# Optimization experiments

Measured on AMD Instinct MI355X. Metric: run time of the kernel, lower is better.

## Reference

```python
import jax, jax.numpy as jnp
import numpy as np

EPS = 1e-5  # torch InstanceNorm2d default eps

def instance_norm(x):
    # per-sample, per-channel normalization over spatial dims (affine=False)
    m = jnp.mean(x, axis=(2, 3), keepdims=True)
    v = jnp.var(x, axis=(2, 3), keepdims=True)
    return (x - m) * jax.lax.rsqrt(v + EPS)

def conv2d(x, w, b, stride, pad):
    y = jax.lax.conv_general_dilated(
        x, w, (stride, stride), [(pad, pad), (pad, pad)],
        dimension_numbers=('NCHW', 'OIHW', 'NCHW'))
    return y + b[None, :, None, None]

def res_block(x, w1, b1, w2, b2):
    out = conv2d(jax.nn.relu(instance_norm(x)), w1, b1, 1, 1)
    out = conv2d(jax.nn.relu(instance_norm(out)), w2, b2, 1, 1)
    return out + x

def res_block_strided(x, w1, b1, w2, b2, ws, bs):
    out = conv2d(jax.nn.relu(instance_norm(x)), w1, b1, 2, 1)
    out = conv2d(jax.nn.relu(instance_norm(out)), w2, b2, 1, 1)
    return out + conv2d(x, ws, bs, 2, 0)  # 1x1 strided skip projection

def setup_inputs() -> dict:
    key = jax.random.key(0)
    ks = jax.random.split(key, 12)
    B, N, C, H, W = 64, 1, 3, 256, 256
    TEXT, EMB, F, HEADS = 256, 512, 32, 5
    FH, FW = H // 16, W // 16  # 16, 16
    def rn(k, shape, scale=0.05):
        return jax.random.normal(k, shape, dtype=jnp.float32) * scale
    z = lambda *s: jnp.zeros(s, jnp.float32)
    return {
        'x': jax.random.normal(ks[0], (B, N, C, H, W), jnp.float32),
        'text_vector': jax.random.normal(ks[1], (B, TEXT), jnp.float32),
        'conv1_w': rn(ks[2], (F, C, 7, 7)),
        'conv1_b': z(F),
        'rbs_w1': rn(ks[3], (3, F, F, 3, 3)),  # 3 strided resblocks
        'rbs_b1': z(3, F),
        'rbs_w2': rn(ks[4], (3, F, F, 3, 3)),
        'rbs_b2': z(3, F),
        'rbs_ws': rn(ks[5], (3, F, F, 1, 1)),
        'rbs_bs': z(3, F),
        'rb_w1': rn(ks[6], (2, F, F, 3, 3)),  # 2 plain resblocks
        'rb_b1': z(2, F),
        'rb_w2': rn(ks[7], (2, F, F, 3, 3)),
        'rb_b2': z(2, F),
        'attn_w': rn(ks[8], (HEADS, FH * FW, TEXT)),  # torch Linear [out,in] per head
        'attn_b': z(HEADS, FH * FW),
        'final_w': rn(ks[9], (EMB, FH * FW * HEADS)),
        'final_b': z(EMB),
    }

def reference(x, text_vector, conv1_w, conv1_b, rbs_w1, rbs_b1, rbs_w2, rbs_b2,
              rbs_ws, rbs_bs, rb_w1, rb_b1, rb_w2, rb_b2, attn_w, attn_b,
              final_w, final_b):
    B, N, C, H, W = x.shape
    feat = x.reshape(B, N * C, H, W)
    feat = instance_norm(feat)
    feat = conv2d(feat, conv1_w, conv1_b, 2, 3)
    # block1 = strided + plain; block2 = strided + plain; block3 = strided
    feat = res_block_strided(feat, rbs_w1[0], rbs_b1[0], rbs_w2[0], rbs_b2[0], rbs_ws[0], rbs_bs[0])
    feat = res_block(feat, rb_w1[0], rb_b1[0], rb_w2[0], rb_b2[0])
    feat = res_block_strided(feat, rbs_w1[1], rbs_b1[1], rbs_w2[1], rbs_b2[1], rbs_ws[1], rbs_bs[1])
    feat = res_block(feat, rb_w1[1], rb_b1[1], rb_w2[1], rb_b2[1])
    feat = res_block_strided(feat, rbs_w1[2], rbs_b1[2], rbs_w2[2], rbs_b2[2], rbs_ws[2], rbs_bs[2])
    # feat: [B, 32, FH, FW]
    HEADS = attn_w.shape[0]
    FH, FW = feat.shape[2], feat.shape[3]
    # sigmoid-gated spatial attention logits per head: [B, HEADS, FH, FW]
    a = jax.nn.sigmoid(jnp.einsum('bt,hot->bho', text_vector, attn_w) + attn_b[None])
    a = a.reshape(B, HEADS, FH, FW)
    # channel scores: spatial sum of gate * feature -> [B, HEADS, C]
    scores = jnp.einsum('bhij,bcij->bhc', a, feat)
    probs = jax.nn.softmax(scores, axis=-1)  # old F.softmax over channel dim
    # weighted channel sum -> per-head attention map [B, HEADS, FH, FW]
    amaps = jnp.einsum('bhc,bcij->bhij', probs, feat)
    out = amaps.reshape(B, -1) @ final_w.T + final_b
    return out
```

## Files before the change

### kernel.cpp

```cpp
#include <hip/hip_runtime.h>
#include <cstdint>
#include <cstddef>

#define INORM_EPS 1e-5f

typedef _Float16 f16;
typedef f16 f16x8 __attribute__((ext_vector_type(8)));
typedef f16 f16x4 __attribute__((ext_vector_type(4)));
typedef float f32x4 __attribute__((ext_vector_type(4)));

__global__ __launch_bounds__(256) void prep(
    const float* __restrict__ rbs_w1, const float* __restrict__ rbs_w2,
    const float* __restrict__ rb_w1, const float* __restrict__ rb_w2,
    const float* __restrict__ rbs_ws, const float* __restrict__ conv1_w,
    float2* __restrict__ SP, f16* __restrict__ wp3, f16* __restrict__ wp1,
    f16* __restrict__ wp7) {
  int i = blockIdx.x * 256 + threadIdx.x;
  if (i < 20672) { SP[i] = make_float2(0.f, 0.f); return; }
  i -= 20672;
  if (i < 92160) {
    int mat = i / 9216, r = i % 9216;
    int p = r >> 10, f = (r >> 9) & 1, l = (r >> 3) & 63, j = r & 7;
    int co = f * 16 + (l & 15), ci = (l >> 4) * 8 + j;
    const float* src; int m;
    if (mat < 3) { src = rbs_w1; m = mat; }
    else if (mat < 6) { src = rbs_w2; m = mat - 3; }
    else if (mat < 8) { src = rb_w1; m = mat - 6; }
    else { src = rb_w2; m = mat - 8; }
    wp3[i] = (f16)src[m * 9216 + co * 288 + ci * 9 + p];
    return;
  }
  i -= 92160;
  if (i < 3072) {
    int mat = i / 1024, r = i % 1024;
    int f = r >> 9, l = (r >> 3) & 63, j = r & 7;
    wp1[i] = (f16)rbs_ws[mat * 1024 + (f * 16 + (l & 15)) * 32 + (l >> 4) * 8 + j];
    return;
  }
  i -= 3072;
  if (i >= 7168) return;
  int ky = i >> 10, f = (i >> 9) & 1, l = (i >> 3) & 63, j = i & 7;
  int k = (l >> 4) * 8 + j, kx = k >> 2, ci = k & 3;
  float v = 0.f;
  if (kx < 7 && ci < 3) v = conv1_w[(f * 16 + (l & 15)) * 147 + ci * 49 + ky * 7 + kx];
  wp7[i] = (f16)v;
}

__global__ __launch_bounds__(256) void stats_raw(const float* __restrict__ in,
                                                 float2* __restrict__ st, int HW) {
  const int map = blockIdx.x >> 3, chunk = blockIdx.x & 7;
  const int n4 = HW >> 5;
  const float4* p = (const float4*)(in + (size_t)map * HW + (size_t)chunk * (HW >> 3));
  float s = 0.f, ss = 0.f;
  for (int i = threadIdx.x; i < n4; i += 256) {
    float4 v = p[i];
    s += v.x + v.y + v.z + v.w;
    ss += v.x * v.x + v.y * v.y + v.z * v.z + v.w * v.w;
  }
  __shared__ float r0[256], r1[256];
  r0[threadIdx.x] = s;
  r1[threadIdx.x] = ss;
  __syncthreads();
  for (int off = 128; off > 0; off >>= 1) {
    if ((int)threadIdx.x < off) {
      r0[threadIdx.x] += r0[threadIdx.x + off];
      r1[threadIdx.x] += r1[threadIdx.x + off];
    }
    __syncthreads();
  }
  if (threadIdx.x == 0) {
    atomicAdd(&st[map].x, r0[0]);
    atomicAdd(&st[map].y, r1[0]);
  }
}

__global__ __launch_bounds__(256) void packx(const float* __restrict__ x,
                                             const float2* __restrict__ SPx,
                                             f16* __restrict__ xP) {
  int u = blockIdx.x * 256 + threadIdx.x;
  if (u >= 262 * 262) return;
  int b = blockIdx.z;
  int r = u / 262, c = u % 262;
  f16x4 out;
  out[0] = (f16)0; out[1] = (f16)0; out[2] = (f16)0; out[3] = (f16)0;
  if (r >= 3 && r < 259 && c >= 3 && c < 259) {
    int ir = r - 3, ic = c - 3;
#pragma unroll
    for (int ci = 0; ci < 3; ci++) {
      float2 s = SPx[b * 3 + ci];
      float mean = s.x * (1.f / 65536.f);
      float rstd = rsqrtf(s.y * (1.f / 65536.f) - mean * mean + INORM_EPS);
      out[ci] = (f16)((x[((size_t)b * 3 + ci) * 65536 + ir * 256 + ic] - mean) * rstd);
    }
  }
  *(f16x4*)(xP + ((size_t)b * 68644 + u) * 4) = out;
}

template <int W, int SKIP>
__global__ __launch_bounds__(256) void conv3r(
    const f16* __restrict__ Rin, const float2* __restrict__ SPin, float inv_hw,
    const f16* __restrict__ wp, const float* __restrict__ bias,
    const float* __restrict__ bias2, const f16* __restrict__ skip,
    const f16* __restrict__ wps, f16* __restrict__ Rout,
    float2* __restrict__ ostats) {
  constexpr int TPR = W / 16;
  constexpr int RPB = 8;
  constexpr int LEN = (RPB * TPR) / 4;
  const int t = threadIdx.x, w = t >> 6, l = t & 63;
  const int n = l & 15, q = l >> 4;
  const int b = blockIdx.z;
  const int tx = w % TPR;
  const int y0 = blockIdx.x * RPB + (w / TPR) * LEN;
  const int x = (tx << 4) + n;
  const f16* Rb = Rin + (size_t)b * W * W * 32;

  f16x8 sc, sh;
#pragma unroll
  for (int j = 0; j < 8; j++) {
    float2 s = SPin[b * 32 + q * 8 + j];
    float mean = s.x * inv_hw;
    float rstd = rsqrtf(s.y * inv_hw - mean * mean + INORM_EPS);
    sc[j] = (f16)rstd;
    sh[j] = (f16)(-mean * rstd);
  }

  f16x8 wf[18];
#pragma unroll
  for (int i = 0; i < 18; i++) wf[i] = *(const f16x8*)(wp + i * 512 + l * 8);
  f16x8 wsf0, wsf1;
  if (SKIP == 2) {
    wsf0 = *(const f16x8*)(wps + l * 8);
    wsf1 = *(const f16x8*)(wps + 512 + l * 8);
  }
  float b0 = bias[n], b1 = bias[16 + n];
  if (SKIP == 2) { b0 += bias2[n]; b1 += bias2[16 + n]; }

  f16* ro = Rout + (size_t)b * W * W * 32;
  const f16* sb = skip ? skip + (size_t)b * (SKIP == 2 ? 4 : 1) * W * W * 32 : nullptr;

  bool okc[3];
#pragma unroll
  for (int kx = 0; kx < 3; kx++) okc[kx] = (unsigned)(x + kx - 1) < (unsigned)W;

  auto rowload = [&](int gy, f16x8* dst) {
    int gyc = min(max(gy, 0), W - 1);
#pragma unroll
    for (int kx = 0; kx < 3; kx++) {
      int gxc = min(max(x + kx - 1, 0), W - 1);
      dst[kx] = *(const f16x8*)(Rb + ((size_t)gyc * W + gxc) * 32 + q * 8);
    }
  };
  auto rownorm = [&](int gy, const f16x8* src, f16x8* dst) {
    bool okr = (unsigned)gy < (unsigned)W;
#pragma unroll
    for (int kx = 0; kx < 3; kx++) {
      f16x8 v = src[kx] * sc + sh;
#pragma unroll
      for (int e = 0; e < 8; e++) v[e] = v[e] > (f16)0 ? v[e] : (f16)0;
      f16x8 z = {};
      dst[kx] = (okr && okc[kx]) ? v : z;
    }
  };

  float sm0 = 0.f, sq0 = 0.f, sm1 = 0.f, sq1 = 0.f;
  f16x8 win[9];
  f16x8 tmp[3], pf[3];
#pragma unroll
  for (int jj = 0; jj < 3; jj++) {
    rowload(y0 + jj - 1, tmp);
    rownorm(y0 + jj - 1, tmp, &win[jj * 3]);
  }

#pragma unroll
  for (int i = 0; i < LEN; i++) {
    int y = y0 + i;
    if (i + 1 < LEN) rowload(y0 + i + 2, pf);
    f32x4 acc0 = {0.f, 0.f, 0.f, 0.f}, acc1 = {0.f, 0.f, 0.f, 0.f};
#pragma unroll
    for (int ky = 0; ky < 3; ky++) {
      int slot = (i + ky) % 3;
#pragma unroll
      for (int kx = 0; kx < 3; kx++) {
        f16x8 a = win[slot * 3 + kx];
        acc0 = __builtin_amdgcn_mfma_f32_16x16x32_f16(a, wf[2 * (ky * 3 + kx)], acc0, 0, 0, 0);
        acc1 = __builtin_amdgcn_mfma_f32_16x16x32_f16(a, wf[2 * (ky * 3 + kx) + 1], acc1, 0, 0, 0);
      }
    }
    if (SKIP == 2) {
      const int Ws = 2 * W;
      f16x8 as = *(const f16x8*)(sb + ((size_t)(2 * y) * Ws + 2 * x) * 32 + q * 8);
      acc0 = __builtin_amdgcn_mfma_f32_16x16x32_f16(as, wsf0, acc0, 0, 0, 0);
      acc1 = __builtin_amdgcn_mfma_f32_16x16x32_f16(as, wsf1, acc1, 0, 0, 0);
    }
#pragma unroll
    for (int r = 0; r < 4; r++) {
      size_t px = (size_t)y * W + (tx << 4) + q * 4 + r;
      float v0 = acc0[r] + b0;
      float v1 = acc1[r] + b1;
      if (SKIP == 1) {
        v0 += (float)sb[px * 32 + n];
        v1 += (float)sb[px * 32 + 16 + n];
      }
      ro[px * 32 + n] = (f16)v0;
      ro[px * 32 + 16 + n] = (f16)v1;
      sm0 += v0; sq0 += v0 * v0;
      sm1 += v1; sq1 += v1 * v1;
    }
    if (i + 1 < LEN) rownorm(y0 + i + 2, pf, &win[(i % 3) * 3]);
  }
  if (ostats) {
    sm0 += __shfl_xor(sm0, 16); sm0 += __shfl_xor(sm0, 32);
    sq0 += __shfl_xor(sq0, 16); sq0 += __shfl_xor(sq0, 32);
    sm1 += __shfl_xor(sm1, 16); sm1 += __shfl_xor(sm1, 32);
    sq1 += __shfl_xor(sq1, 16); sq1 += __shfl_xor(sq1, 32);
    if (l < 16) {
      atomicAdd(&ostats[b * 32 + n].x, sm0);
      atomicAdd(&ostats[b * 32 + n].y, sq0);
      atomicAdd(&ostats[b * 32 + 16 + n].x, sm1);
      atomicAdd(&ostats[b * 32 + 16 + n].y, sq1);
    }
  }
}

template <int WIN, int STRIDE, int SKIP>
__global__ __launch_bounds__(256) void conv3n(
    const f16* __restrict__ Rin, const float2* __restrict__ SPin, float inv_hw,
    const f16* __restrict__ wp, const float* __restrict__ bias,
    const float* __restrict__ bias2, const f16* __restrict__ skip,
    const f16* __restrict__ wps, f16* __restrict__ Rout,
    float2* __restrict__ ostats) {
  constexpr int WOUT = WIN / STRIDE;
  constexpr int TPR = WOUT / 16;
  constexpr int RPB = (WOUT >= 32) ? 4 : 8;
  constexpr int UNITS = TPR * RPB;
  constexpr int U = UNITS / 4;
  const int t = threadIdx.x, w = t >> 6, l = t & 63;
  const int n = l & 15, q = l >> 4;
  const int b = blockIdx.z;
  const int yb = blockIdx.x * RPB;
  const f16* Rb = Rin + (size_t)b * WIN * WIN * 32;

  f16x8 sc, sh;
#pragma unroll
  for (int j = 0; j < 8; j++) {
    float2 s = SPin[b * 32 + q * 8 + j];
    float mean = s.x * inv_hw;
    float rstd = rsqrtf(s.y * inv_hw - mean * mean + INORM_EPS);
    sc[j] = (f16)rstd;
    sh[j] = (f16)(-mean * rstd);
  }

  f16x8 wf[18];
#pragma unroll
  for (int i = 0; i < 18; i++) wf[i] = *(const f16x8*)(wp + i * 512 + l * 8);
  f16x8 wsf0, wsf1;
  if (SKIP == 2) {
    wsf0 = *(const f16x8*)(wps + l * 8);
    wsf1 = *(const f16x8*)(wps + 512 + l * 8);
  }
  float b0 = bias[n], b1 = bias[16 + n];
  if (SKIP == 2) { b0 += bias2[n]; b1 += bias2[16 + n]; }

  f16* ro = Rout + (size_t)b * WOUT * WOUT * 32;
  const f16* sb = skip ? skip + (size_t)b * (SKIP == 2 ? 4 : 1) * WOUT * WOUT * 32 : nullptr;

  auto load_u = [&](int u, f16x8* a) {
    int ty = u / TPR, tx = u % TPR;
    int y = yb + ty;
#pragma unroll
    for (int kx = 0; kx < 3; kx++) {
      int gx = STRIDE * ((tx << 4) + n) + kx - 1;
      int gxc = min(max(gx, 0), WIN - 1);
#pragma unroll
      for (int ky = 0; ky < 3; ky++) {
        int gy = STRIDE * y + ky - 1;
        int gyc = min(max(gy, 0), WIN - 1);
        a[ky * 3 + kx] = *(const f16x8*)(Rb + ((size_t)gyc * WIN + gxc) * 32 + q * 8);
      }
    }
  };
  auto norm_u = [&](int u, f16x8* a) {
    int ty = u / TPR, tx = u % TPR;
    int y = yb + ty;
#pragma unroll
    for (int kx = 0; kx < 3; kx++) {
      int gx = STRIDE * ((tx << 4) + n) + kx - 1;
      bool okx = (unsigned)gx < (unsigned)WIN;
#pragma unroll
      for (int ky = 0; ky < 3; ky++) {
        int gy = STRIDE * y + ky - 1;
        bool ok = okx && ((unsigned)gy < (unsigned)WIN);
        f16x8 v = a[ky * 3 + kx] * sc + sh;
#pragma unroll
        for (int e = 0; e < 8; e++) v[e] = v[e] > (f16)0 ? v[e] : (f16)0;
        f16x8 z = {};
        a[ky * 3 + kx] = ok ? v : z;
      }
    }
  };

  float sm0 = 0.f, sq0 = 0.f, sm1 = 0.f, sq1 = 0.f;
  f16x8 araw[9], anxt[9];
  load_u(w, araw);
#pragma unroll
  for (int i = 0; i < U; i++) {
    int u = w + 4 * i;
    if (i + 1 < U) load_u(u + 4, anxt);
    norm_u(u, araw);
    int ty = u / TPR, tx = u % TPR;
    int y = yb + ty, x0 = tx << 4;
    f32x4 acc0 = {0.f, 0.f, 0.f, 0.f}, acc1 = {0.f, 0.f, 0.f, 0.f};
#pragma unroll
    for (int p = 0; p < 9; p++) {
      acc0 = __builtin_amdgcn_mfma_f32_16x16x32_f16(araw[p], wf[2 * p], acc0, 0, 0, 0);
      acc1 = __builtin_amdgcn_mfma_f32_16x16x32_f16(araw[p], wf[2 * p + 1], acc1, 0, 0, 0);
    }
    if (SKIP == 2) {
      const int Ws = 2 * WOUT;
      f16x8 as = *(const f16x8*)(sb + ((size_t)(2 * y) * Ws + 2 * (x0 + n)) * 32 + q * 8);
      acc0 = __builtin_amdgcn_mfma_f32_16x16x32_f16(as, wsf0, acc0, 0, 0, 0);
      acc1 = __builtin_amdgcn_mfma_f32_16x16x32_f16(as, wsf1, acc1, 0, 0, 0);
    }
#pragma unroll
    for (int r = 0; r < 4; r++) {
      size_t px = (size_t)y * WOUT + x0 + q * 4 + r;
      float v0 = acc0[r] + b0;
      float v1 = acc1[r] + b1;
      if (SKIP == 1) {
        v0 += (float)sb[px * 32 + n];
        v1 += (float)sb[px * 32 + 16 + n];
      }
      ro[px * 32 + n] = (f16)v0;
      ro[px * 32 + 16 + n] = (f16)v1;
      sm0 += v0; sq0 += v0 * v0;
      sm1 += v1; sq1 += v1 * v1;
    }
#pragma unroll
    for (int p = 0; p < 9; p++) araw[p] = anxt[p];
  }
  if (ostats) {
    sm0 += __shfl_xor(sm0, 16); sm0 += __shfl_xor(sm0, 32);
    sq0 += __shfl_xor(sq0, 16); sq0 += __shfl_xor(sq0, 32);
    sm1 += __shfl_xor(sm1, 16); sm1 += __shfl_xor(sm1, 32);
    sq1 += __shfl_xor(sq1, 16); sq1 += __shfl_xor(sq1, 32);
    if (l < 16) {
      atomicAdd(&ostats[b * 32 + n].x, sm0);
      atomicAdd(&ostats[b * 32 + n].y, sq0);
      atomicAdd(&ostats[b * 32 + 16 + n].x, sm1);
      atomicAdd(&ostats[b * 32 + 16 + n].y, sq1);
    }
  }
}

__global__ __launch_bounds__(256) void conv7(
    const f16* __restrict__ xP, const f16* __restrict__ wp,
    const float* __restrict__ bias, f16* __restrict__ Rout,
    float2* __restrict__ ostats) {
  const int t = threadIdx.x, w = t >> 6, l = t & 63;
  const int n = l & 15, q = l >> 4;
  const int b = blockIdx.z;
  const int yb = blockIdx.x * 8;
  const f16* Xb = xP + (size_t)b * 68644 * 4;
  f16x8 wf[14];
#pragma unroll
  for (int i = 0; i < 14; i++) wf[i] = *(const f16x8*)(wp + i * 512 + l * 8);
  float b0 = bias[n], b1 = bias[16 + n];
  float sm0 = 0.f, sq0 = 0.f, sm1 = 0.f, sq1 = 0.f;
  f16* ro = Rout + (size_t)b * 16384 * 32;

#pragma unroll
  for (int seg = 0; seg < 2; seg++) {
    const int tx = w + seg * 4;
    const int x0 = tx * 16;
    const f16* base = Xb + (size_t)(2 * (x0 + n) + 2 * q) * 4;
    f16x8 win[7];
#pragma unroll
    for (int j = 0; j < 7; j++)
      win[j] = *(const f16x8*)(base + (size_t)(2 * yb + j) * 1048);
    f16x8 pf0, pf1;
#pragma unroll
    for (int i = 0; i < 8; i++) {
      if (i < 7) {
        pf0 = *(const f16x8*)(base + (size_t)(2 * yb + 2 * i + 7) * 1048);
        pf1 = *(const f16x8*)(base + (size_t)(2 * yb + 2 * i + 8) * 1048);
      }
      int y = yb + i;
      f32x4 acc0 = {0.f, 0.f, 0.f, 0.f}, acc1 = {0.f, 0.f, 0.f, 0.f};
#pragma unroll
      for (int ky = 0; ky < 7; ky++) {
        f16x8 a = win[(2 * i + ky) % 7];
        acc0 = __builtin_amdgcn_mfma_f32_16x16x32_f16(a, wf[2 * ky], acc0, 0, 0, 0);
        acc1 = __builtin_amdgcn_mfma_f32_16x16x32_f16(a, wf[2 * ky + 1], acc1, 0, 0, 0);
      }
#pragma unroll
      for (int r = 0; r < 4; r++) {
        size_t px = (size_t)y * 128 + x0 + q * 4 + r;
        float v0 = acc0[r] + b0;
        float v1 = acc1[r] + b1;
        ro[px * 32 + n] = (f16)v0;
        ro[px * 32 + 16 + n] = (f16)v1;
        sm0 += v0; sq0 += v0 * v0;
        sm1 += v1; sq1 += v1 * v1;
      }
      if (i < 7) {
        win[(2 * i) % 7] = pf0;
        win[(2 * i + 1) % 7] = pf1;
      }
    }
  }
  sm0 += __shfl_xor(sm0, 16); sm0 += __shfl_xor(sm0, 32);
  sq0 += __shfl_xor(sq0, 16); sq0 += __shfl_xor(sq0, 32);
  sm1 += __shfl_xor(sm1, 16); sm1 += __shfl_xor(sm1, 32);
  sq1 += __shfl_xor(sq1, 16); sq1 += __shfl_xor(sq1, 32);
  if (l < 16) {
    atomicAdd(&ostats[b * 32 + n].x, sm0);
    atomicAdd(&ostats[b * 32 + n].y, sq0);
    atomicAdd(&ostats[b * 32 + 16 + n].x, sm1);
    atomicAdd(&ostats[b * 32 + 16 + n].y, sq1);
  }
}

__global__ __launch_bounds__(256) void gates_kernel(
    const float* __restrict__ text, const float* __restrict__ attn_w,
    const float* __restrict__ attn_b, float* __restrict__ G) {
  __shared__ float s_text[64 * 257];
  __shared__ float s_w[16 * 256];
  const int t = threadIdx.x, wv = t >> 6, lane = t & 63;
  const int o0 = blockIdx.x * 16;
  for (int d = t; d < 16384; d += 256) {
    int b = d >> 8, k = d & 255;
    s_text[b * 257 + k] = text[d];
  }
  for (int d = t; d < 4096; d += 256) s_w[d] = attn_w[(size_t)o0 * 256 + d];
  __syncthreads();
  float acc[4];
#pragma unroll
  for (int j = 0; j < 4; j++) acc[j] = attn_b[o0 + wv * 4 + j];
  for (int k = 0; k < 256; k++) {
    float tv = s_text[lane * 257 + k];
#pragma unroll
    for (int j = 0; j < 4; j++) acc[j] = fmaf(s_w[(wv * 4 + j) * 256 + k], tv, acc[j]);
  }
#pragma unroll
  for (int j = 0; j < 4; j++) {
    int o = o0 + wv * 4 + j;
    G[o * 64 + lane] = 1.f / (1.f + __expf(-acc[j]));
  }
}

__global__ __launch_bounds__(256) void scores_kernel(
    const f16* __restrict__ feat, const float* __restrict__ G,
    float* __restrict__ amapT) {
  __shared__ float s_feat[256 * 33];
  __shared__ float s_gate[1280];
  __shared__ float s_scores[5 * 32];
  __shared__ float s_probs[5 * 32];
  const int b = blockIdx.x;
  const int t = threadIdx.x;

  for (int i = t; i < 8192; i += 256)
    s_feat[(i >> 5) * 33 + (i & 31)] = (float)feat[(size_t)b * 8192 + i];
  for (int i = t; i < 1280; i += 256) s_gate[i] = G[i * 64 + b];
  __syncthreads();

  if (t < 160) {
    int h = t >> 5, c = t & 31;
    float acc = 0.f;
    for (int ij = 0; ij < 256; ij++) acc += s_gate[h * 256 + ij] * s_feat[ij * 33 + c];
    s_scores[t] = acc;
  }
  __syncthreads();

  if (t < 5) {
    float mx = -1e30f;
    for (int c = 0; c < 32; c++) mx = fmaxf(mx, s_scores[t * 32 + c]);
    float sum = 0.f;
    for (int c = 0; c < 32; c++) {
      float e = __expf(s_scores[t * 32 + c] - mx);
      s_probs[t * 32 + c] = e;
      sum += e;
    }
    float inv = 1.f / sum;
    for (int c = 0; c < 32; c++) s_probs[t * 32 + c] *= inv;
  }
  __syncthreads();

  for (int h = 0; h < 5; h++) {
    float acc = 0.f;
    for (int c = 0; c < 32; c++) acc += s_probs[h * 32 + c] * s_feat[t * 33 + c];
    amapT[(h * 256 + t) * 64 + b] = acc;
  }
}

__global__ __launch_bounds__(256) void final_kernel(
    const float* __restrict__ amapT, const float* __restrict__ final_w,
    const float* __restrict__ final_b, float* __restrict__ out) {
  __shared__ float s_w[4 * 1280];
  __shared__ float s_red[4][4][64];
  const int t = threadIdx.x, wv = t >> 6, lane = t & 63;
  const int e0 = blockIdx.x * 4;
  for (int d = t; d < 5120; d += 256) s_w[d] = final_w[(size_t)e0 * 1280 + d];
  __syncthreads();
  const int k0 = wv * 320;
  float acc[4] = {0.f, 0.f, 0.f, 0.f};
  for (int k = k0; k < k0 + 320; k++) {
    float av = amapT[k * 64 + lane];
#pragma unroll
    for (int e = 0; e < 4; e++) acc[e] = fmaf(s_w[e * 1280 + k], av, acc[e]);
  }
#pragma unroll
  for (int e = 0; e < 4; e++) s_red[wv][e][lane] = acc[e];
  __syncthreads();
  if (wv == 0) {
#pragma unroll
    for (int e = 0; e < 4; e++) {
      float v = s_red[0][e][lane] + s_red[1][e][lane] + s_red[2][e][lane] +
                s_red[3][e][lane] + final_b[e0 + e];
      out[(size_t)lane * 512 + e0 + e] = v;
    }
  }
}

extern "C" void kernel_launch(void* const* d_in, const int* in_sizes, int n_in,
                              void* d_out, int out_size, void* d_ws, size_t ws_size,
                              hipStream_t stream) {
  (void)in_sizes; (void)n_in; (void)out_size; (void)ws_size;
  const float* x       = (const float*)d_in[0];
  const float* text    = (const float*)d_in[1];
  const float* conv1_w = (const float*)d_in[2];
  const float* conv1_b = (const float*)d_in[3];
  const float* rbs_w1  = (const float*)d_in[4];
  const float* rbs_b1  = (const float*)d_in[5];
  const float* rbs_w2  = (const float*)d_in[6];
  const float* rbs_b2  = (const float*)d_in[7];
  const float* rbs_ws  = (const float*)d_in[8];
  const float* rbs_bs  = (const float*)d_in[9];
  const float* rb_w1   = (const float*)d_in[10];
  const float* rb_b1   = (const float*)d_in[11];
  const float* rb_w2   = (const float*)d_in[12];
  const float* rb_b2   = (const float*)d_in[13];
  const float* attn_w  = (const float*)d_in[14];
  const float* attn_b  = (const float*)d_in[15];
  const float* final_w = (const float*)d_in[16];
  const float* final_b = (const float*)d_in[17];
  float* out = (float*)d_out;

  char* wsb = (char*)d_ws;
  f16*   xP   = (f16*)(wsb + 0);
  f16*   R128 = (f16*)(wsb + 35145728);
  f16*   R64a = (f16*)(wsb + 102254592);
  f16*   R64b = (f16*)(wsb + 119031808);
  f16*   R64c = (f16*)(wsb + 135809024);
  f16*   R32a = (f16*)(wsb + 152586240);
  f16*   R32b = (f16*)(wsb + 156780544);
  f16*   R32c = (f16*)(wsb + 160974848);
  f16*   R16a = (f16*)(wsb + 165169152);
  f16*   R16b = (f16*)(wsb + 166217728);
  float2* SP  = (float2*)(wsb + 167266304);
  float2* SPx = (float2*)(wsb + 167430144);
  f16*   wp3  = (f16*)(wsb + 167431680);
  f16*   wp1  = (f16*)(wsb + 167616000);
  f16*   wp7  = (f16*)(wsb + 167622144);
  float* G     = (float*)(wsb + 167636480);
  float* amapT = (float*)(wsb + 167964160);
  float2* SP0 = SP + 0 * 2048;
  float2* SP1 = SP + 1 * 2048;
  float2* SP2 = SP + 2 * 2048;
  float2* SP3 = SP + 3 * 2048;
  float2* SP4 = SP + 4 * 2048;
  float2* SP5 = SP + 5 * 2048;
  float2* SP6 = SP + 6 * 2048;
  float2* SP7 = SP + 7 * 2048;
  float2* SP8 = SP + 8 * 2048;
  float2* SP9 = SP + 9 * 2048;

  prep<<<481, 256, 0, stream>>>(rbs_w1, rbs_w2, rb_w1, rb_w2, rbs_ws, conv1_w,
                                SP, wp3, wp1, wp7);
  stats_raw<<<1536, 256, 0, stream>>>(x, SPx, 65536);
  packx<<<dim3(269, 1, 64), 256, 0, stream>>>(x, SPx, xP);

  conv7<<<dim3(16, 1, 64), 256, 0, stream>>>(xP, wp7, conv1_b, R128, SP0);

  conv3n<128, 2, 0><<<dim3(16, 1, 64), 256, 0, stream>>>(
      R128, SP0, 1.f / 16384.f, wp3, rbs_b1, nullptr, nullptr, nullptr, R64a, SP1);
  conv3r<64, 2><<<dim3(8, 1, 64), 256, 0, stream>>>(
      R64a, SP1, 1.f / 4096.f, wp3 + 3 * 9216, rbs_b2, rbs_bs, R128, wp1, R64b, SP2);

  conv3r<64, 0><<<dim3(8, 1, 64), 256, 0, stream>>>(
      R64b, SP2, 1.f / 4096.f, wp3 + 6 * 9216, rb_b1, nullptr, nullptr, nullptr, R64c, SP3);
  conv3r<64, 1><<<dim3(8, 1, 64), 256, 0, stream>>>(
      R64c, SP3, 1.f / 4096.f, wp3 + 8 * 9216, rb_b2, nullptr, R64b, nullptr, R64a, SP4);

  conv3n<64, 2, 0><<<dim3(8, 1, 64), 256, 0, stream>>>(
      R64a, SP4, 1.f / 4096.f, wp3 + 1 * 9216, rbs_b1 + 32, nullptr, nullptr, nullptr, R32a, SP5);
  conv3r<32, 2><<<dim3(4, 1, 64), 256, 0, stream>>>(
      R32a, SP5, 1.f / 1024.f, wp3 + 4 * 9216, rbs_b2 + 32, rbs_bs + 32, R64a, wp1 + 1024, R32b, SP6);

  conv3r<32, 0><<<dim3(4, 1, 64), 256, 0, stream>>>(
      R32b, SP6, 1.f / 1024.f, wp3 + 7 * 9216, rb_b1 + 32, nullptr, nullptr, nullptr, R32c, SP7);
  conv3r<32, 1><<<dim3(4, 1, 64), 256, 0, stream>>>(
      R32c, SP7, 1.f / 1024.f, wp3 + 9 * 9216, rb_b2 + 32, nullptr, R32b, nullptr, R32a, SP8);

  conv3n<32, 2, 0><<<dim3(2, 1, 64), 256, 0, stream>>>(
      R32a, SP8, 1.f / 1024.f, wp3 + 2 * 9216, rbs_b1 + 64, nullptr, nullptr, nullptr, R16a, SP9);
  conv3n<16, 1, 2><<<dim3(2, 1, 64), 256, 0, stream>>>(
      R16a, SP9, 1.f / 256.f, wp3 + 5 * 9216, rbs_b2 + 64, rbs_bs + 64, R32a, wp1 + 2048, R16b, nullptr);

  gates_kernel<<<80, 256, 0, stream>>>(text, attn_w, attn_b, G);
  scores_kernel<<<64, 256, 0, stream>>>(R16b, G, amapT);
  final_kernel<<<128, 256, 0, stream>>>(amapT, final_w, final_b, out);
}
```

Measured before the change: 324.3 us.

## Fuse input normalization into conv7 and add register-windowed stride-2 conv kernel

Removes the packx kernel. conv7 now reads the raw fp32 input directly, applies instance-norm and zero padding in registers, and converts to f16 on the fly. This saves a full write and reread of the padded f16 image, but conv7 now does scattered scalar fp32 loads. It also adds a conv3s2 kernel for the stride-2 3x3 convs that keeps a rolling 3-row register window with prefetch and fused norm+ReLU, replacing the generic conv3n path with a different launch grid.

```diff
diff --git a/kernel.cpp b/kernel.cpp
--- a/kernel.cpp
+++ b/kernel.cpp
@@ -6,7 +6,6 @@
 
 typedef _Float16 f16;
 typedef f16 f16x8 __attribute__((ext_vector_type(8)));
-typedef f16 f16x4 __attribute__((ext_vector_type(4)));
 typedef float f32x4 __attribute__((ext_vector_type(4)));
 
 __global__ __launch_bounds__(256) void prep(
@@ -74,28 +73,6 @@
   }
 }
 
-__global__ __launch_bounds__(256) void packx(const float* __restrict__ x,
-                                             const float2* __restrict__ SPx,
-                                             f16* __restrict__ xP) {
-  int u = blockIdx.x * 256 + threadIdx.x;
-  if (u >= 262 * 262) return;
-  int b = blockIdx.z;
-  int r = u / 262, c = u % 262;
-  f16x4 out;
-  out[0] = (f16)0; out[1] = (f16)0; out[2] = (f16)0; out[3] = (f16)0;
-  if (r >= 3 && r < 259 && c >= 3 && c < 259) {
-    int ir = r - 3, ic = c - 3;
-#pragma unroll
-    for (int ci = 0; ci < 3; ci++) {
-      float2 s = SPx[b * 3 + ci];
-      float mean = s.x * (1.f / 65536.f);
-      float rstd = rsqrtf(s.y * (1.f / 65536.f) - mean * mean + INORM_EPS);
-      out[ci] = (f16)((x[((size_t)b * 3 + ci) * 65536 + ir * 256 + ic] - mean) * rstd);
-    }
-  }
-  *(f16x4*)(xP + ((size_t)b * 68644 + u) * 4) = out;
-}
-
 template <int W, int SKIP>
 __global__ __launch_bounds__(256) void conv3r(
     const f16* __restrict__ Rin, const float2* __restrict__ SPin, float inv_hw,
@@ -222,6 +199,119 @@
   }
 }
 
+template <int WIN>
+__global__ __launch_bounds__(256) void conv3s2(
+    const f16* __restrict__ Rin, const float2* __restrict__ SPin, float inv_hw,
+    const f16* __restrict__ wp, const float* __restrict__ bias,
+    f16* __restrict__ Rout, float2* __restrict__ ostats) {
+  constexpr int WOUT = WIN / 2;
+  constexpr int TPR = WOUT / 16;
+  constexpr int RPB = 8;
+  constexpr int LEN = (RPB * TPR) / 4;
+  const int t = threadIdx.x, w = t >> 6, l = t & 63;
+  const int n = l & 15, q = l >> 4;
+  const int b = blockIdx.z;
+  const int tx = w % TPR;
+  const int y0 = blockIdx.x * RPB + (w / TPR) * LEN;
+  const int x = (tx << 4) + n;
+  const f16* Rb = Rin + (size_t)b * WIN * WIN * 32;
+
+  f16x8 sc, sh;
+#pragma unroll
+  for (int j = 0; j < 8; j++) {
+    float2 s = SPin[b * 32 + q * 8 + j];
+    float mean = s.x * inv_hw;
+    float rstd = rsqrtf(s.y * inv_hw - mean * mean + INORM_EPS);
+    sc[j] = (f16)rstd;
+    sh[j] = (f16)(-mean * rstd);
+  }
+
+  f16x8 wf[18];
+#pragma unroll
+  for (int i = 0; i < 18; i++) wf[i] = *(const f16x8*)(wp + i * 512 + l * 8);
+  float b0 = bias[n], b1 = bias[16 + n];
+
+  f16* ro = Rout + (size_t)b * WOUT * WOUT * 32;
+
+  bool okc[3];
+#pragma unroll
+  for (int kx = 0; kx < 3; kx++) okc[kx] = (unsigned)(2 * x + kx - 1) < (unsigned)WIN;
+
+  auto rowload = [&](int gy, f16x8* dst) {
+    int gyc = min(max(gy, 0), WIN - 1);
+#pragma unroll
+    for (int kx = 0; kx < 3; kx++) {
+      int gxc = min(max(2 * x + kx - 1, 0), WIN - 1);
+      dst[kx] = *(const f16x8*)(Rb + ((size_t)gyc * WIN + gxc) * 32 + q * 8);
+    }
+  };
+  auto rownorm = [&](int gy, const f16x8* src, f16x8* dst) {
+    bool okr = (unsigned)gy < (unsigned)WIN;
+#pragma unroll
+    for (int kx = 0; kx < 3; kx++) {
+      f16x8 v = src[kx] * sc + sh;
+#pragma unroll
+      for (int e = 0; e < 8; e++) v[e] = v[e] > (f16)0 ? v[e] : (f16)0;
+      f16x8 z = {};
+      dst[kx] = (okr && okc[kx]) ? v : z;
+    }
+  };
+
+  float sm0 = 0.f, sq0 = 0.f, sm1 = 0.f, sq1 = 0.f;
+  f16x8 win[9], pa[3], pb[3];
+#pragma unroll
+  for (int jj = 0; jj < 3; jj++) {
+    rowload(2 * y0 - 1 + jj, pa);
+    rownorm(2 * y0 - 1 + jj, pa, &win[jj * 3]);
+  }
+
+#pragma unroll
+  for (int i = 0; i < LEN; i++) {
+    int y = y0 + i;
+    if (i + 1 < LEN) {
+      rowload(2 * y + 2, pa);
+      rowload(2 * y + 3, pb);
+    }
+    f32x4 acc0 = {0.f, 0.f, 0.f, 0.f}, acc1 = {0.f, 0.f, 0.f, 0.f};
+#pragma unroll
+    for (int ky = 0; ky < 3; ky++) {
+      int slot = (2 * i + ky) % 3;
+#pragma unroll
+      for (int kx = 0; kx < 3; kx++) {
+        f16x8 a = win[slot * 3 + kx];
+        acc0 = __builtin_amdgcn_mfma_f32_16x16x32_f16(a, wf[2 * (ky * 3 + kx)], acc0, 0, 0, 0);
+        acc1 = __builtin_amdgcn_mfma_f32_16x16x32_f16(a, wf[2 * (ky * 3 + kx) + 1], acc1, 0, 0, 0);
+      }
+    }
+#pragma unroll
+    for (int r = 0; r < 4; r++) {
+      size_t px = (size_t)y * WOUT + (tx << 4) + q * 4 + r;
+      float v0 = acc0[r] + b0;
+      float v1 = acc1[r] + b1;
+      ro[px * 32 + n] = (f16)v0;
+      ro[px * 32 + 16 + n] = (f16)v1;
+      sm0 += v0; sq0 += v0 * v0;
+      sm1 += v1; sq1 += v1 * v1;
+    }
+    if (i + 1 < LEN) {
+      rownorm(2 * y + 2, pa, &win[((2 * i + 3) % 3) * 3]);
+      rownorm(2 * y + 3, pb, &win[((2 * i + 4) % 3) * 3]);
+    }
+  }
+  if (ostats) {
+    sm0 += __shfl_xor(sm0, 16); sm0 += __shfl_xor(sm0, 32);
+    sq0 += __shfl_xor(sq0, 16); sq0 += __shfl_xor(sq0, 32);
+    sm1 += __shfl_xor(sm1, 16); sm1 += __shfl_xor(sm1, 32);
+    sq1 += __shfl_xor(sq1, 16); sq1 += __shfl_xor(sq1, 32);
+    if (l < 16) {
+      atomicAdd(&ostats[b * 32 + n].x, sm0);
+      atomicAdd(&ostats[b * 32 + n].y, sq0);
+      atomicAdd(&ostats[b * 32 + 16 + n].x, sm1);
+      atomicAdd(&ostats[b * 32 + 16 + n].y, sq1);
+    }
+  }
+}
+
 template <int WIN, int STRIDE, int SKIP>
 __global__ __launch_bounds__(256) void conv3n(
     const f16* __restrict__ Rin, const float2* __restrict__ SPin, float inv_hw,
@@ -353,14 +443,21 @@
 }
 
 __global__ __launch_bounds__(256) void conv7(
-    const f16* __restrict__ xP, const f16* __restrict__ wp,
-    const float* __restrict__ bias, f16* __restrict__ Rout,
-    float2* __restrict__ ostats) {
+    const float* __restrict__ x, const float2* __restrict__ SPx,
+    const f16* __restrict__ wp, const float* __restrict__ bias,
+    f16* __restrict__ Rout, float2* __restrict__ ostats) {
   const int t = threadIdx.x, w = t >> 6, l = t & 63;
   const int n = l & 15, q = l >> 4;
   const int b = blockIdx.z;
   const int yb = blockIdx.x * 8;
-  const f16* Xb = xP + (size_t)b * 68644 * 4;
+  const float* Xb = x + (size_t)b * 3 * 65536;
+  float mn[3], rs[3];
+#pragma unroll
+  for (int ci = 0; ci < 3; ci++) {
+    float2 s = SPx[b * 3 + ci];
+    mn[ci] = s.x * (1.f / 65536.f);
+    rs[ci] = rsqrtf(s.y * (1.f / 65536.f) - mn[ci] * mn[ci] + INORM_EPS);
+  }
   f16x8 wf[14];
 #pragma unroll
   for (int i = 0; i < 14; i++) wf[i] = *(const f16x8*)(wp + i * 512 + l * 8);
@@ -372,17 +469,48 @@
   for (int seg = 0; seg < 2; seg++) {
     const int tx = w + seg * 4;
     const int x0 = tx * 16;
-    const f16* base = Xb + (size_t)(2 * (x0 + n) + 2 * q) * 4;
+    const int c0 = 2 * (x0 + n) + 2 * q - 3, c1 = c0 + 1;
+    const bool v0 = (unsigned)c0 < 256u, v1 = (unsigned)c1 < 256u;
+    const int cc0 = v0 ? c0 : 0, cc1 = v1 ? c1 : 0;
+
+    auto ld6 = [&](int r, float* u) -> bool {
+      bool okr = (unsigned)r < 256u;
+      const float* p = Xb + (size_t)(okr ? r : 0) * 256;
+#pragma unroll
+      for (int ci = 0; ci < 3; ci++) {
+        u[ci] = p[ci * 65536 + cc0];
+        u[3 + ci] = p[ci * 65536 + cc1];
+      }
+      return okr;
+    };
+    auto fin = [&](bool okr, const float* u, f16x8& a) {
+      f16x8 r = {};
+#pragma unroll
+      for (int ci = 0; ci < 3; ci++) {
+        float g0 = (u[ci] - mn[ci]) * rs[ci];
+        float g1 = (u[3 + ci] - mn[ci]) * rs[ci];
+        r[ci] = (okr && v0) ? (f16)g0 : (f16)0;
+        r[4 + ci] = (okr && v1) ? (f16)g1 : (f16)0;
+      }
+      a = r;
+    };
+
     f16x8 win[7];
-#pragma unroll
-    for (int j = 0; j < 7; j++)
-      win[j] = *(const f16x8*)(base + (size_t)(2 * yb + j) * 1048);
-    f16x8 pf0, pf1;
+    {
+      float u[6];
+#pragma unroll
+      for (int j = 0; j < 7; j++) {
+        bool ok = ld6(2 * yb + j - 3, u);
+        fin(ok, u, win[j]);
+      }
+    }
+    float ua[6], ub[6];
+    bool oA = false, oB = false;
 #pragma unroll
     for (int i = 0; i < 8; i++) {
       if (i < 7) {
-        pf0 = *(const f16x8*)(base + (size_t)(2 * yb + 2 * i + 7) * 1048);
-        pf1 = *(const f16x8*)(base + (size_t)(2 * yb + 2 * i + 8) * 1048);
+        oA = ld6(2 * yb + 2 * i + 4, ua);
+        oB = ld6(2 * yb + 2 * i + 5, ub);
       }
       int y = yb + i;
       f32x4 acc0 = {0.f, 0.f, 0.f, 0.f}, acc1 = {0.f, 0.f, 0.f, 0.f};
@@ -395,16 +523,16 @@
 #pragma unroll
       for (int r = 0; r < 4; r++) {
         size_t px = (size_t)y * 128 + x0 + q * 4 + r;
-        float v0 = acc0[r] + b0;
-        float v1 = acc1[r] + b1;
-        ro[px * 32 + n] = (f16)v0;
-        ro[px * 32 + 16 + n] = (f16)v1;
-        sm0 += v0; sq0 += v0 * v0;
-        sm1 += v1; sq1 += v1 * v1;
+        float v0r = acc0[r] + b0;
+        float v1r = acc1[r] + b1;
+        ro[px * 32 + n] = (f16)v0r;
+        ro[px * 32 + 16 + n] = (f16)v1r;
+        sm0 += v0r; sq0 += v0r * v0r;
+        sm1 += v1r; sq1 += v1r * v1r;
       }
       if (i < 7) {
-        win[(2 * i) % 7] = pf0;
-        win[(2 * i + 1) % 7] = pf1;
+        fin(oA, ua, win[(2 * i) % 7]);
+        fin(oB, ub, win[(2 * i + 1) % 7]);
       }
     }
   }
@@ -546,7 +674,6 @@
   float* out = (float*)d_out;
 
   char* wsb = (char*)d_ws;
-  f16*   xP   = (f16*)(wsb + 0);
   f16*   R128 = (f16*)(wsb + 35145728);
   f16*   R64a = (f16*)(wsb + 102254592);
   f16*   R64b = (f16*)(wsb + 119031808);
@@ -577,12 +704,11 @@
   prep<<<481, 256, 0, stream>>>(rbs_w1, rbs_w2, rb_w1, rb_w2, rbs_ws, conv1_w,
                                 SP, wp3, wp1, wp7);
   stats_raw<<<1536, 256, 0, stream>>>(x, SPx, 65536);
-  packx<<<dim3(269, 1, 64), 256, 0, stream>>>(x, SPx, xP);
-
-  conv7<<<dim3(16, 1, 64), 256, 0, stream>>>(xP, wp7, conv1_b, R128, SP0);
-
-  conv3n<128, 2, 0><<<dim3(16, 1, 64), 256, 0, stream>>>(
-      R128, SP0, 1.f / 16384.f, wp3, rbs_b1, nullptr, nullptr, nullptr, R64a, SP1);
+
+  conv7<<<dim3(16, 1, 64), 256, 0, stream>>>(x, SPx, wp7, conv1_b, R128, SP0);
+
+  conv3s2<128><<<dim3(8, 1, 64), 256, 0, stream>>>(
+      R128, SP0, 1.f / 16384.f, wp3, rbs_b1, R64a, SP1);
   conv3r<64, 2><<<dim3(8, 1, 64), 256, 0, stream>>>(
       R64a, SP1, 1.f / 4096.f, wp3 + 3 * 9216, rbs_b2, rbs_bs, R128, wp1, R64b, SP2);
 
@@ -591,8 +717,8 @@
   conv3r<64, 1><<<dim3(8, 1, 64), 256, 0, stream>>>(
       R64c, SP3, 1.f / 4096.f, wp3 + 8 * 9216, rb_b2, nullptr, R64b, nullptr, R64a, SP4);
 
-  conv3n<64, 2, 0><<<dim3(8, 1, 64), 256, 0, stream>>>(
-      R64a, SP4, 1.f / 4096.f, wp3 + 1 * 9216, rbs_b1 + 32, nullptr, nullptr, nullptr, R32a, SP5);
+  conv3s2<64><<<dim3(4, 1, 64), 256, 0, stream>>>(
+      R64a, SP4, 1.f / 4096.f, wp3 + 1 * 9216, rbs_b1 + 32, R32a, SP5);
   conv3r<32, 2><<<dim3(4, 1, 64), 256, 0, stream>>>(
       R32a, SP5, 1.f / 1024.f, wp3 + 4 * 9216, rbs_b2 + 32, rbs_bs + 32, R64a, wp1 + 1024, R32b, SP6);
 
@@ -601,8 +727,8 @@
   conv3r<32, 1><<<dim3(4, 1, 64), 256, 0, stream>>>(
       R32c, SP7, 1.f / 1024.f, wp3 + 9 * 9216, rb_b2 + 32, nullptr, R32b, nullptr, R32a, SP8);
 
-  conv3n<32, 2, 0><<<dim3(2, 1, 64), 256, 0, stream>>>(
-      R32a, SP8, 1.f / 1024.f, wp3 + 2 * 9216, rbs_b1 + 64, nullptr, nullptr, nullptr, R16a, SP9);
+  conv3s2<32><<<dim3(2, 1, 64), 256, 0, stream>>>(
+      R32a, SP8, 1.f / 1024.f, wp3 + 2 * 9216, rbs_b1 + 64, R16a, SP9);
   conv3n<16, 1, 2><<<dim3(2, 1, 64), 256, 0, stream>>>(
       R16a, SP9, 1.f / 256.f, wp3 + 5 * 9216, rbs_b2 + 64, rbs_bs + 64, R32a, wp1 + 2048, R16b, nullptr);
 
```

Measured after the change: 504.8 us. +55.7%, slower.

## Fuse input normalization and padding into conv7 via LDS staging

Applied to the files above, without the earlier changes.

Removes the separate packx kernel that wrote a padded, normalized fp16 copy of the input to global memory. conv7 now reads the raw fp32 input, normalizes it with the precomputed stats, and stages a 21-row halo tile in shared memory, feeding the MFMA operands from LDS instead of a register prefetch window. This saves one kernel launch and a global write and read of the packed input. In exchange, halo rows are loaded redundantly across blocks, the input reads are uncoalesced strided fp32, and a block-wide sync plus about 44 KB of LDS may reduce occupancy.

```diff
diff --git a/kernel.cpp b/kernel.cpp
--- a/kernel.cpp
+++ b/kernel.cpp
@@ -74,28 +74,6 @@
   }
 }
 
-__global__ __launch_bounds__(256) void packx(const float* __restrict__ x,
-                                             const float2* __restrict__ SPx,
-                                             f16* __restrict__ xP) {
-  int u = blockIdx.x * 256 + threadIdx.x;
-  if (u >= 262 * 262) return;
-  int b = blockIdx.z;
-  int r = u / 262, c = u % 262;
-  f16x4 out;
-  out[0] = (f16)0; out[1] = (f16)0; out[2] = (f16)0; out[3] = (f16)0;
-  if (r >= 3 && r < 259 && c >= 3 && c < 259) {
-    int ir = r - 3, ic = c - 3;
-#pragma unroll
-    for (int ci = 0; ci < 3; ci++) {
-      float2 s = SPx[b * 3 + ci];
-      float mean = s.x * (1.f / 65536.f);
-      float rstd = rsqrtf(s.y * (1.f / 65536.f) - mean * mean + INORM_EPS);
-      out[ci] = (f16)((x[((size_t)b * 3 + ci) * 65536 + ir * 256 + ic] - mean) * rstd);
-    }
-  }
-  *(f16x4*)(xP + ((size_t)b * 68644 + u) * 4) = out;
-}
-
 template <int W, int SKIP>
 __global__ __launch_bounds__(256) void conv3r(
     const f16* __restrict__ Rin, const float2* __restrict__ SPin, float inv_hw,
@@ -353,18 +331,42 @@
 }
 
 __global__ __launch_bounds__(256) void conv7(
-    const f16* __restrict__ xP, const f16* __restrict__ wp,
-    const float* __restrict__ bias, f16* __restrict__ Rout,
-    float2* __restrict__ ostats) {
+    const float* __restrict__ x, const float2* __restrict__ SPx,
+    const f16* __restrict__ wp, const float* __restrict__ bias,
+    f16* __restrict__ Rout, float2* __restrict__ ostats) {
+  __shared__ f16 lds[21 * 131 * 8];
   const int t = threadIdx.x, w = t >> 6, l = t & 63;
   const int n = l & 15, q = l >> 4;
   const int b = blockIdx.z;
   const int yb = blockIdx.x * 8;
-  const f16* Xb = xP + (size_t)b * 68644 * 4;
+  const float* Xb = x + (size_t)b * 3 * 65536;
+  float mn[3], rs[3];
+#pragma unroll
+  for (int ci = 0; ci < 3; ci++) {
+    float2 s = SPx[b * 3 + ci];
+    mn[ci] = s.x * (1.f / 65536.f);
+    rs[ci] = rsqrtf(s.y * (1.f / 65536.f) - mn[ci] * mn[ci] + INORM_EPS);
+  }
   f16x8 wf[14];
 #pragma unroll
   for (int i = 0; i < 14; i++) wf[i] = *(const f16x8*)(wp + i * 512 + l * 8);
   float b0 = bias[n], b1 = bias[16 + n];
+
+  for (int idx = t; idx < 21 * 262; idx += 256) {
+    int ri = idx / 262, cl = idx - ri * 262;
+    int row = 2 * yb - 3 + ri, col = cl - 3;
+    bool ok = ((unsigned)row < 256u) && ((unsigned)col < 256u);
+    f16x4 v = {};
+    if (ok) {
+      const float* p = Xb + (size_t)row * 256 + col;
+      v[0] = (f16)((p[0] - mn[0]) * rs[0]);
+      v[1] = (f16)((p[65536] - mn[1]) * rs[1]);
+      v[2] = (f16)((p[131072] - mn[2]) * rs[2]);
+    }
+    *(f16x4*)(lds + ((ri * 131 + (cl >> 1)) * 8) + (cl & 1) * 4) = v;
+  }
+  __syncthreads();
+
   float sm0 = 0.f, sq0 = 0.f, sm1 = 0.f, sq1 = 0.f;
   f16* ro = Rout + (size_t)b * 16384 * 32;
 
@@ -372,23 +374,14 @@
   for (int seg = 0; seg < 2; seg++) {
     const int tx = w + seg * 4;
     const int x0 = tx * 16;
-    const f16* base = Xb + (size_t)(2 * (x0 + n) + 2 * q) * 4;
-    f16x8 win[7];
-#pragma unroll
-    for (int j = 0; j < 7; j++)
-      win[j] = *(const f16x8*)(base + (size_t)(2 * yb + j) * 1048);
-    f16x8 pf0, pf1;
+    const int u = x0 + n + q;
 #pragma unroll
     for (int i = 0; i < 8; i++) {
-      if (i < 7) {
-        pf0 = *(const f16x8*)(base + (size_t)(2 * yb + 2 * i + 7) * 1048);
-        pf1 = *(const f16x8*)(base + (size_t)(2 * yb + 2 * i + 8) * 1048);
-      }
       int y = yb + i;
       f32x4 acc0 = {0.f, 0.f, 0.f, 0.f}, acc1 = {0.f, 0.f, 0.f, 0.f};
 #pragma unroll
       for (int ky = 0; ky < 7; ky++) {
-        f16x8 a = win[(2 * i + ky) % 7];
+        f16x8 a = *(const f16x8*)(lds + ((2 * i + ky) * 131 + u) * 8);
         acc0 = __builtin_amdgcn_mfma_f32_16x16x32_f16(a, wf[2 * ky], acc0, 0, 0, 0);
         acc1 = __builtin_amdgcn_mfma_f32_16x16x32_f16(a, wf[2 * ky + 1], acc1, 0, 0, 0);
       }
@@ -401,10 +394,6 @@
         ro[px * 32 + 16 + n] = (f16)v1;
         sm0 += v0; sq0 += v0 * v0;
         sm1 += v1; sq1 += v1 * v1;
-      }
-      if (i < 7) {
-        win[(2 * i) % 7] = pf0;
-        win[(2 * i + 1) % 7] = pf1;
       }
     }
   }
@@ -546,7 +535,6 @@
   float* out = (float*)d_out;
 
   char* wsb = (char*)d_ws;
-  f16*   xP   = (f16*)(wsb + 0);
   f16*   R128 = (f16*)(wsb + 35145728);
   f16*   R64a = (f16*)(wsb + 102254592);
   f16*   R64b = (f16*)(wsb + 119031808);
@@ -577,9 +565,8 @@
   prep<<<481, 256, 0, stream>>>(rbs_w1, rbs_w2, rb_w1, rb_w2, rbs_ws, conv1_w,
                                 SP, wp3, wp1, wp7);
   stats_raw<<<1536, 256, 0, stream>>>(x, SPx, 65536);
-  packx<<<dim3(269, 1, 64), 256, 0, stream>>>(x, SPx, xP);
-
-  conv7<<<dim3(16, 1, 64), 256, 0, stream>>>(xP, wp7, conv1_b, R128, SP0);
+
+  conv7<<<dim3(16, 1, 64), 256, 0, stream>>>(x, SPx, wp7, conv1_b, R128, SP0);
 
   conv3n<128, 2, 0><<<dim3(16, 1, 64), 256, 0, stream>>>(
       R128, SP0, 1.f / 16384.f, wp3, rbs_b1, nullptr, nullptr, nullptr, R64a, SP1);
```

New measurement: 453.7 us. +39.9%, slower.
